# Kernel optimization log

Hardware: AMD Instinct MI355X
Metric: run time of the kernel (lower is better)

The kernel has to match this reference:

```python
import jax, jax.numpy as jnp
import numpy as np

DIM = 512
NUM_HEADS = 8
HEAD_DIM = DIM // NUM_HEADS
GAMMA = 1.0


def setup_inputs() -> dict:
    key = jax.random.key(0)
    ks = jax.random.split(key, 10)
    B, S = 2, 2048
    x_real = jax.random.normal(ks[0], (B, S, DIM), dtype=jnp.float32)
    x_imag = jax.random.normal(ks[1], (B, S, DIM), dtype=jnp.float32)
    def xavier(k, fan_in, fan_out):
        lim = float(np.sqrt(6.0 / (fan_in + fan_out)))
        return jax.random.uniform(k, (fan_in, fan_out), jnp.float32, -lim, lim)
    # torch Linear(in,out): weight [out,in]; we store transposed [in,out]
    Wq = xavier(ks[2], 2 * DIM, DIM); bq = jnp.zeros((DIM,), jnp.float32)
    Wk = xavier(ks[3], 2 * DIM, DIM); bk = jnp.zeros((DIM,), jnp.float32)
    Wv = xavier(ks[4], 2 * DIM, DIM); bv = jnp.zeros((DIM,), jnp.float32)
    Wo = xavier(ks[5], DIM, 2 * DIM); bo = jnp.zeros((2 * DIM,), jnp.float32)
    return {"x_real": x_real, "x_imag": x_imag, "Wq": Wq, "bq": bq,
            "Wk": Wk, "bk": bk, "Wv": Wv, "bv": bv, "Wo": Wo, "bo": bo}


def reference(x_real, x_imag, Wq, bq, Wk, bk, Wv, bv, Wo, bo):
    B, S, _ = x_real.shape
    real_embed = jnp.concatenate([x_real, x_imag], axis=-1)  # [B,S,2*dim]
    def proj(W, b):
        y = real_embed @ W + b                               # [B,S,dim]
        return y.reshape(B, S, NUM_HEADS, HEAD_DIM).transpose(0, 2, 1, 3)  # [B,H,S,d]
    Q = proj(Wq, bq)
    K = proj(Wk, bk)
    V = proj(Wv, bv)
    # softmax over head_dim is broadcast-invariant, so the Bhattacharyya
    # coefficient sum_d sqrt(p_i[d]*q_j[d]) factorizes into a matmul.
    sp = jnp.sqrt(jax.nn.softmax(Q, axis=-1))  # [B,H,S,d]
    sq = jnp.sqrt(jax.nn.softmax(K, axis=-1))  # [B,H,S,d]
    bc = jnp.einsum('bhid,bhjd->bhij', sp, sq)  # Bhattacharyya coeff [B,H,S,S]
    bc = jnp.clip(bc, -1.0, 1.0)
    dist = jnp.arccos(bc)
    attn = jax.nn.softmax(-GAMMA * dist * dist, axis=-1)  # [B,H,S,S]
    attended = jnp.einsum('bhij,bhjd->bhid', attn, V)
    attended = attended.transpose(0, 2, 1, 3).reshape(B, S, DIM)
    out = attended @ Wo + bo  # [B,S,2*dim] = concat(real_out, imag_out)
    return out
```

## Files before the change

### kernel.cpp

```cpp
#include <hip/hip_runtime.h>
#include <math.h>


typedef __attribute__((ext_vector_type(8))) short short8;
typedef __attribute__((ext_vector_type(4))) short bf16x4;
typedef __attribute__((ext_vector_type(4))) float f32x4;
typedef __attribute__((ext_vector_type(2))) float f32x2;

#define MFMA(a, b, c) __builtin_amdgcn_mfma_f32_16x16x32_bf16((a), (b), (c), 0, 0, 0)

static __device__ __forceinline__ short f2bf(float f) {
    unsigned u = __float_as_uint(f);
    u += 0x7fffu + ((u >> 16) & 1u);
    return (short)(u >> 16);
}

static __device__ __forceinline__ void gld_lds16(const short* g, short* l) {
    __builtin_amdgcn_global_load_lds(
        (const __attribute__((address_space(1))) unsigned int*)g,
        (__attribute__((address_space(3))) unsigned int*)l, 16, 0, 0);
}

__global__ __launch_bounds__(256) void convert_x(
    const float* __restrict__ xr, const float* __restrict__ xi,
    short* __restrict__ xb)
{
    int idx = blockIdx.x * 256 + threadIdx.x;
    int e = idx << 2;
    int m = e >> 10, k = e & 1023;
    const float* src = (k < 512) ? xr : xi;
    float4 t = *(const float4*)(src + (size_t)m * 512 + (k & 511));
    unsigned lo = (unsigned short)f2bf(t.x) | ((unsigned)(unsigned short)f2bf(t.y) << 16);
    unsigned hi = (unsigned short)f2bf(t.z) | ((unsigned)(unsigned short)f2bf(t.w) << 16);
    uint2 o; o.x = lo; o.y = hi;
    *(uint2*)(xb + e) = o;
}

__global__ __launch_bounds__(256) void transpose_w(
    const float* __restrict__ Wq, const float* __restrict__ Wk,
    const float* __restrict__ Wv, const float* __restrict__ Wo,
    short* __restrict__ wqt, short* __restrict__ wkt,
    short* __restrict__ wvt, short* __restrict__ wot)
{
    __shared__ float t[32][33];
    const int z = blockIdx.z;
    const float* src = (z == 0) ? Wq : (z == 1) ? Wk : (z == 2) ? Wv : Wo;
    short* dst = (z == 0) ? wqt : (z == 1) ? wkt : (z == 2) ? wvt : wot;
    const int K = (z < 3) ? 1024 : 512;
    const int N = (z < 3) ? 512 : 1024;
    const int n0 = blockIdx.x << 5, k0 = blockIdx.y << 5;
    if (n0 >= N || k0 >= K) return;
    const int tx = threadIdx.x & 31, ty = threadIdx.x >> 5;
    #pragma unroll
    for (int i = 0; i < 4; ++i)
        t[ty + 8 * i][tx] = src[(size_t)(k0 + ty + 8 * i) * N + n0 + tx];
    __syncthreads();
    #pragma unroll
    for (int i = 0; i < 4; ++i)
        dst[(size_t)(n0 + ty + 8 * i) * K + k0 + tx] = f2bf(t[tx][ty + 8 * i]);
}

__global__ __launch_bounds__(128, 4) void qkv_mfma(
    const short* __restrict__ xb, const short* __restrict__ wcat,
    const float* __restrict__ bq, const float* __restrict__ bk,
    const float* __restrict__ bv,
    short* __restrict__ sp, short* __restrict__ sq, short* __restrict__ vt)
{
    __shared__ short As[2][128 * 32];
    __shared__ short Bs[2][64 * 32];
    const int jb = blockIdx.x;
    const int m0 = blockIdx.y << 7;
    const int tid = threadIdx.x;
    const int w = tid >> 6, lane = tid & 63;
    const int l = lane & 15, quad = lane >> 4;

    const int srow = lane >> 2;
    const int sseg = (lane & 3) << 3;
    const short* gA = xb   + (size_t)(m0        + (w << 6) + srow) * 1024 + sseg;
    const short* gB = wcat + (size_t)((jb << 6) + (w << 5) + srow) * 1024 + sseg;

    #pragma unroll
    for (int t = 0; t < 4; ++t)
        gld_lds16(gA + t * 16 * 1024, &As[0][((w << 2) + t) << 9]);
    #pragma unroll
    for (int t = 0; t < 2; ++t)
        gld_lds16(gB + t * 16 * 1024, &Bs[0][((w << 1) + t) << 9]);
    __syncthreads();

    const f32x4 z4 = {0.f, 0.f, 0.f, 0.f};
    f32x4 acc[4][4];
    #pragma unroll
    for (int i = 0; i < 4; ++i)
        #pragma unroll
        for (int j = 0; j < 4; ++j) acc[i][j] = z4;

    for (int kt = 0; kt < 32; ++kt) {
        const int cb = kt & 1, nb = cb ^ 1;
        if (kt < 31) {
            const int k0 = (kt + 1) << 5;
            #pragma unroll
            for (int t = 0; t < 4; ++t)
                gld_lds16(gA + k0 + t * 16 * 1024, &As[nb][((w << 2) + t) << 9]);
            #pragma unroll
            for (int t = 0; t < 2; ++t)
                gld_lds16(gB + k0 + t * 16 * 1024, &Bs[nb][((w << 1) + t) << 9]);
        }
        const short* Al = &As[cb][(w << 6) << 5];
        const short* Bl = &Bs[cb][0];
        short8 af[4], bfr[4];
        #pragma unroll
        for (int i = 0; i < 4; ++i)
            af[i] = *(const short8*)(Al + (((i << 4) + l) << 5) + (quad << 3));
        #pragma unroll
        for (int j = 0; j < 4; ++j)
            bfr[j] = *(const short8*)(Bl + (((j << 4) + l) << 5) + (quad << 3));
        #pragma unroll
        for (int i = 0; i < 4; ++i)
            #pragma unroll
            for (int j = 0; j < 4; ++j)
                acc[i][j] = MFMA(af[i], bfr[j], acc[i][j]);
        __syncthreads();
    }

    const int op = jb >> 3;
    const int h  = jb & 7;

    if (op < 2) {
        short* dst = (op == 0) ? sp : sq;
        const float* bias = (op == 0) ? bq : bk;
        float bcol[4];
        #pragma unroll
        for (int nt = 0; nt < 4; ++nt) bcol[nt] = bias[(h << 6) + (nt << 4) + l];
        #pragma unroll
        for (int i = 0; i < 4; ++i) {
            #pragma unroll
            for (int reg = 0; reg < 4; ++reg) {
                const int r = m0 + (w << 6) + (i << 4) + (quad << 2) + reg;
                const int b = r >> 11, s = r & 2047;
                float v[4];
                #pragma unroll
                for (int nt = 0; nt < 4; ++nt) v[nt] = acc[i][nt][reg] + bcol[nt];
                float mx = fmaxf(fmaxf(v[0], v[1]), fmaxf(v[2], v[3]));
                #pragma unroll
                for (int msk = 1; msk < 16; msk <<= 1) mx = fmaxf(mx, __shfl_xor(mx, msk));
                float e[4], ssum = 0.f;
                #pragma unroll
                for (int nt = 0; nt < 4; ++nt) { e[nt] = __expf(v[nt] - mx); ssum += e[nt]; }
                #pragma unroll
                for (int msk = 1; msk < 16; msk <<= 1) ssum += __shfl_xor(ssum, msk);
                float inv = 1.0f / ssum;
                short* o = dst + ((size_t)((b << 3) + h) * 2048 + s) * 64 + l;
                #pragma unroll
                for (int nt = 0; nt < 4; ++nt)
                    o[nt << 4] = f2bf(sqrtf(e[nt] * inv));
            }
        }
    } else {
        float bcol[4];
        #pragma unroll
        for (int nt = 0; nt < 4; ++nt) bcol[nt] = bv[(h << 6) + (nt << 4) + l];
        #pragma unroll
        for (int i = 0; i < 4; ++i) {
            const int sb = m0 + (w << 6) + (i << 4) + (quad << 2);
            const int b = sb >> 11, s = sb & 2047;
            #pragma unroll
            for (int nt = 0; nt < 4; ++nt) {
                const int d = (nt << 4) + l;
                bf16x4 pk;
                #pragma unroll
                for (int reg = 0; reg < 4; ++reg)
                    pk[reg] = f2bf(acc[i][nt][reg] + bcol[nt]);
                *(bf16x4*)(vt + ((size_t)((b << 3) + h) * 64 + d) * 2048 + s) = pk;
            }
        }
    }
}

__global__ __launch_bounds__(256, 4) void attn_mfma(
    const short* __restrict__ sp, const short* __restrict__ sq,
    const short* __restrict__ vt, short* __restrict__ attB)
{
    __shared__ __align__(16) short sqT[2][64 * 64];
    __shared__ __align__(16) short vtT[2][64 * 64];
    __shared__ __align__(16) short Pb[4][16 * 64];
    __shared__ float denB[4][16];
    const int bh = blockIdx.y;
    const int m0 = blockIdx.x << 6;
    const int tid = threadIdx.x;
    const int w = tid >> 6, lane = tid & 63;
    const int l = lane & 15, quad = lane >> 4;
    const int l7 = l & 7;

    const short* spB = sp + (size_t)bh * 2048 * 64;
    const short* sqB = sq + (size_t)bh * 2048 * 64;
    const short* vtB = vt + (size_t)bh * 64 * 2048;

    const short* apr = spB + (size_t)(m0 + w * 16 + l) * 64 + quad * 8;
    short8 aq0 = *(const short8*)(apr);
    short8 aq1 = *(const short8*)(apr + 32);
    short8 nq0 = aq0 ^ (short)0x8000;
    short8 nq1 = aq1 ^ (short)0x8000;

    const int srow = tid >> 2;
    const int scol = (tid & 3) * 16;
    const short* sqG = sqB + (size_t)srow * 64 + scol;
    const short* vtG = vtB + (size_t)srow * 2048 + scol;
    const int sl0 = (tid & 3) << 1;
    const int sw0 = srow * 64 + (((sl0    ) ^ (srow & 7)) << 3);
    const int sw1 = srow * 64 + (((sl0 | 1) ^ (srow & 7)) << 3);

    const int sRd = (quad ^ l7) << 3;

    {
        short8 a0 = *(const short8*)(sqG);
        short8 a1 = *(const short8*)(sqG + 8);
        short8 b0 = *(const short8*)(vtG);
        short8 b1 = *(const short8*)(vtG + 8);
        *(short8*)(&sqT[0][sw0]) = a0;
        *(short8*)(&sqT[0][sw1]) = a1;
        *(short8*)(&vtT[0][sw0]) = b0;
        *(short8*)(&vtT[0][sw1]) = b1;
    }
    __syncthreads();

    const f32x4 z4 = {0.f, 0.f, 0.f, 0.f};
    const f32x4 ones4 = {1.f, 1.f, 1.f, 1.f};
    f32x4 acc[4] = {z4, z4, z4, z4};
    f32x2 den2 = {0.f, 0.f};
    short* Pw = &Pb[w][0];

    #pragma unroll 1
    for (int jt = 0; jt < 32; ++jt) {
        const int cb = jt & 1, nb = cb ^ 1;
        const int j0n = ((jt + 1) & 31) << 6;
        short8 na0 = *(const short8*)(sqG + (size_t)j0n * 64);
        short8 na1 = *(const short8*)(sqG + (size_t)j0n * 64 + 8);
        short8 nb0 = *(const short8*)(vtG + j0n);
        short8 nb1 = *(const short8*)(vtG + j0n + 8);

        const short* sqL = &sqT[cb][0];
        #pragma unroll
        for (int nt = 0; nt < 4; ++nt) {
            const short* ar = sqL + ((nt * 16 + l) << 6);
            short8 sa0 = *(const short8*)(ar + sRd);
            short8 sa1 = *(const short8*)(ar + (sRd ^ 32));
            f32x4 p = MFMA(sa0, nq0, ones4);
            p = MFMA(sa1, nq1, p);
            f32x2 u01 = {p[0], p[1]};
            f32x2 u23 = {p[2], p[3]};
            const f32x2 zz = {0.f, 0.f};
#if __has_builtin(__builtin_elementwise_max)
            u01 = __builtin_elementwise_max(u01, zz);
            u23 = __builtin_elementwise_max(u23, zz);
#else
            u01.x = fmaxf(u01.x, 0.f); u01.y = fmaxf(u01.y, 0.f);
            u23.x = fmaxf(u23.x, 0.f); u23.y = fmaxf(u23.y, 0.f);
#endif
            f32x2 t01 = {0.000922f, 0.000922f};
            f32x2 t23 = t01;
            t01 = t01 * u01 + 0.00152228f;  t23 = t23 * u23 + 0.00152228f;
            t01 = t01 * u01 + 0.00384801f;  t23 = t23 * u23 + 0.00384801f;
            t01 = t01 * u01 + 0.01015873f;  t23 = t23 * u23 + 0.01015873f;
            t01 = t01 * u01 + 0.02857143f;  t23 = t23 * u23 + 0.02857143f;
            t01 = t01 * u01 + 0.08888889f;  t23 = t23 * u23 + 0.08888889f;
            t01 = t01 * u01 + 0.33333333f;  t23 = t23 * u23 + 0.33333333f;
            t01 = t01 * u01 + 2.0f;         t23 = t23 * u23 + 2.0f;
            f32x2 w01 = u01 * t01;
            f32x2 w23 = u23 * t23;
            float e0 = __expf(-w01.x), e1 = __expf(-w01.y);
            float e2 = __expf(-w23.x), e3 = __expf(-w23.y);
            f32x2 es = {e0 + e2, e1 + e3};
            den2 += es;
            uint2 pk;
            pk.x = (__float_as_uint(e0) >> 16) | (__float_as_uint(e1) & 0xffff0000u);
            pk.y = (__float_as_uint(e2) >> 16) | (__float_as_uint(e3) & 0xffff0000u);
            *(uint2*)(&Pw[(l << 6) + ((((nt << 1) + (quad >> 1)) ^ l7) << 3)
                          + ((quad & 1) << 2)]) = pk;
        }

        const short* pr = Pw + (l << 6);
        short8 pa0 = *(const short8*)(pr + sRd);
        short8 pa1 = *(const short8*)(pr + (sRd ^ 32));
        const short* vL = &vtT[cb][0];
        #pragma unroll
        for (int t4 = 0; t4 < 4; ++t4) {
            const short* vr = vL + ((t4 * 16 + l) << 6);
            short8 vb0 = *(const short8*)(vr + sRd);
            short8 vb1 = *(const short8*)(vr + (sRd ^ 32));
            acc[t4] = MFMA(pa0, vb0, acc[t4]);
            acc[t4] = MFMA(pa1, vb1, acc[t4]);
        }

        *(short8*)(&sqT[nb][sw0]) = na0;
        *(short8*)(&sqT[nb][sw1]) = na1;
        *(short8*)(&vtT[nb][sw0]) = nb0;
        *(short8*)(&vtT[nb][sw1]) = nb1;
        __syncthreads();
    }

    float den = den2.x + den2.y;
    den += __shfl_xor(den, 16);
    den += __shfl_xor(den, 32);
    if (lane < 16) denB[w][l] = den;
    float invd[4];
    #pragma unroll
    for (int reg = 0; reg < 4; ++reg)
        invd[reg] = 1.0f / denB[w][quad * 4 + reg];

    const int b = bh >> 3, hh = bh & 7;
    #pragma unroll
    for (int t4 = 0; t4 < 4; ++t4)
        #pragma unroll
        for (int reg = 0; reg < 4; ++reg) {
            const int row = m0 + w * 16 + quad * 4 + reg;
            attB[((size_t)(b * 2048 + row)) * 512 + hh * 64 + t4 * 16 + l] =
                f2bf(acc[t4][reg] * invd[reg]);
        }
}

__global__ __launch_bounds__(256, 3) void out_mfma(
    const short* __restrict__ attB, const short* __restrict__ wot,
    const float* __restrict__ bo, float* __restrict__ out)
{
    __shared__ short As[2][128 * 32];
    __shared__ short Bs[2][64 * 32];
    const int nb0 = blockIdx.x << 6;
    const int m0 = blockIdx.y << 7;
    const int tid = threadIdx.x;
    const int w = tid >> 6, lane = tid & 63;
    const int l = lane & 15, quad = lane >> 4;

    const short* gA = attB + (size_t)(m0  + (w << 4) + (lane >> 2)) * 512 + ((lane & 3) << 3);
    const short* gB = wot  + (size_t)(nb0 + (w << 4) + (lane >> 2)) * 512 + ((lane & 3) << 3);

    gld_lds16(gA,            &As[0][w << 9]);
    gld_lds16(gA + 64 * 512, &As[0][(w + 4) << 9]);
    gld_lds16(gB,            &Bs[0][w << 9]);
    __syncthreads();

    const f32x4 z4 = {0.f, 0.f, 0.f, 0.f};
    f32x4 acc[4][2];
    #pragma unroll
    for (int i = 0; i < 4; ++i) { acc[i][0] = z4; acc[i][1] = z4; }

    const int rsel = (w >> 1) << 6;
    const int csel = (w & 1) << 5;

    for (int kt = 0; kt < 16; ++kt) {
        const int cb = kt & 1, nbuf = cb ^ 1;
        if (kt < 15) {
            const int k0 = (kt + 1) << 5;
            gld_lds16(gA + k0,            &As[nbuf][w << 9]);
            gld_lds16(gA + k0 + 64 * 512, &As[nbuf][(w + 4) << 9]);
            gld_lds16(gB + k0,            &Bs[nbuf][w << 9]);
        }
        const short* Al = &As[cb][rsel << 5];
        const short* Bl = &Bs[cb][csel << 5];
        short8 af[4], bfr[2];
        #pragma unroll
        for (int i = 0; i < 4; ++i)
            af[i] = *(const short8*)(Al + (((i << 4) + l) << 5) + (quad << 3));
        #pragma unroll
        for (int j = 0; j < 2; ++j)
            bfr[j] = *(const short8*)(Bl + (((j << 4) + l) << 5) + (quad << 3));
        #pragma unroll
        for (int i = 0; i < 4; ++i) {
            acc[i][0] = MFMA(af[i], bfr[0], acc[i][0]);
            acc[i][1] = MFMA(af[i], bfr[1], acc[i][1]);
        }
        __syncthreads();
    }

    const int n0 = nb0 + csel;
    float bcol[2];
    bcol[0] = bo[n0 + l];
    bcol[1] = bo[n0 + 16 + l];
    #pragma unroll
    for (int i = 0; i < 4; ++i)
        #pragma unroll
        for (int reg = 0; reg < 4; ++reg) {
            const int m = m0 + rsel + (i << 4) + (quad << 2) + reg;
            float* o = out + (size_t)m * 1024 + n0 + l;
            o[0]  = acc[i][0][reg] + bcol[0];
            o[16] = acc[i][1][reg] + bcol[1];
        }
}

extern "C" void kernel_launch(void* const* d_in, const int* in_sizes, int n_in,
                              void* d_out, int out_size, void* d_ws, size_t ws_size,
                              hipStream_t stream) {
    const float* xr = (const float*)d_in[0];
    const float* xi = (const float*)d_in[1];
    const float* Wq = (const float*)d_in[2];
    const float* bq = (const float*)d_in[3];
    const float* Wk = (const float*)d_in[4];
    const float* bk = (const float*)d_in[5];
    const float* Wv = (const float*)d_in[6];
    const float* bv = (const float*)d_in[7];
    const float* Wo = (const float*)d_in[8];
    const float* bo = (const float*)d_in[9];
    float* out = (float*)d_out;

    short* base = (short*)d_ws;
    short* xb   = base;
    short* wqt  = xb  + 4194304;
    short* wkt  = wqt + 524288;
    short* wvt  = wkt + 524288;
    short* wot  = wvt + 524288;
    short* spW  = wot + 524288;
    short* sqW  = spW + 2097152;
    short* vtW  = sqW + 2097152;
    short* attB = vtW + 2097152;

    hipLaunchKernelGGL(convert_x, dim3(4096), dim3(256), 0, stream, xr, xi, xb);
    hipLaunchKernelGGL(transpose_w, dim3(32, 32, 4), dim3(256), 0, stream,
                       Wq, Wk, Wv, Wo, wqt, wkt, wvt, wot);
    hipLaunchKernelGGL(qkv_mfma, dim3(24, 32), dim3(128), 0, stream,
                       xb, wqt, bq, bk, bv, spW, sqW, vtW);
    hipLaunchKernelGGL(attn_mfma, dim3(32, 16), dim3(256), 0, stream,
                       spW, sqW, vtW, attB);
    hipLaunchKernelGGL(out_mfma, dim3(16, 32), dim3(256), 0, stream,
                       attB, wot, bo, out);
}
```

Baseline: 185.7 us.

## Triple-buffer LDS staging in QKV and output GEMMs with partial vmcnt waits

Both projection GEMMs move from double to triple-buffered global-to-LDS loads. Each iteration issues loads two k-tiles ahead and waits only for the older batch (vmcnt) before a raw barrier, instead of a full __syncthreads drain. The goal is to hide global load latency behind MFMA work. It raises LDS use per block, which may reduce occupancy. It also issues wasted wrap-around loads in the last two iterations and relies on hand-counted vmcnt values being correct.

New measurement: 185.5 us. No clear change (-0.1%).

```diff
diff --git a/kernel.cpp b/kernel.cpp
--- a/kernel.cpp
+++ b/kernel.cpp
@@ -66,8 +66,8 @@
     const float* __restrict__ bv,
     short* __restrict__ sp, short* __restrict__ sq, short* __restrict__ vt)
 {
-    __shared__ short As[2][128 * 32];
-    __shared__ short Bs[2][64 * 32];
+    __shared__ short As[3][128 * 32];
+    __shared__ short Bs[3][64 * 32];
     const int jb = blockIdx.x;
     const int m0 = blockIdx.y << 7;
     const int tid = threadIdx.x;
@@ -79,13 +79,20 @@
     const short* gA = xb   + (size_t)(m0        + (w << 6) + srow) * 1024 + sseg;
     const short* gB = wcat + (size_t)((jb << 6) + (w << 5) + srow) * 1024 + sseg;
 
-    #pragma unroll
-    for (int t = 0; t < 4; ++t)
-        gld_lds16(gA + t * 16 * 1024, &As[0][((w << 2) + t) << 9]);
-    #pragma unroll
-    for (int t = 0; t < 2; ++t)
-        gld_lds16(gB + t * 16 * 1024, &Bs[0][((w << 1) + t) << 9]);
-    __syncthreads();
+    auto STAGE = [&](int bb, int kk) {
+        const int k0 = kk << 5;
+        #pragma unroll
+        for (int t = 0; t < 4; ++t)
+            gld_lds16(gA + k0 + t * 16 * 1024, &As[bb][((w << 2) + t) << 9]);
+        #pragma unroll
+        for (int t = 0; t < 2; ++t)
+            gld_lds16(gB + k0 + t * 16 * 1024, &Bs[bb][((w << 1) + t) << 9]);
+    };
+
+    STAGE(0, 0);
+    STAGE(1, 1);
+    asm volatile("s_waitcnt vmcnt(6)" ::: "memory");
+    __builtin_amdgcn_s_barrier();
 
     const f32x4 z4 = {0.f, 0.f, 0.f, 0.f};
     f32x4 acc[4][4];
@@ -94,17 +101,10 @@
         #pragma unroll
         for (int j = 0; j < 4; ++j) acc[i][j] = z4;
 
+    int cb = 0, sb = 2;
+    #pragma unroll 1
     for (int kt = 0; kt < 32; ++kt) {
-        const int cb = kt & 1, nb = cb ^ 1;
-        if (kt < 31) {
-            const int k0 = (kt + 1) << 5;
-            #pragma unroll
-            for (int t = 0; t < 4; ++t)
-                gld_lds16(gA + k0 + t * 16 * 1024, &As[nb][((w << 2) + t) << 9]);
-            #pragma unroll
-            for (int t = 0; t < 2; ++t)
-                gld_lds16(gB + k0 + t * 16 * 1024, &Bs[nb][((w << 1) + t) << 9]);
-        }
+        STAGE(sb, (kt + 2) & 31);
         const short* Al = &As[cb][(w << 6) << 5];
         const short* Bl = &Bs[cb][0];
         short8 af[4], bfr[4];
@@ -119,8 +119,12 @@
             #pragma unroll
             for (int j = 0; j < 4; ++j)
                 acc[i][j] = MFMA(af[i], bfr[j], acc[i][j]);
-        __syncthreads();
+        asm volatile("s_waitcnt vmcnt(6)" ::: "memory");
+        __builtin_amdgcn_s_barrier();
+        cb = (cb == 2) ? 0 : cb + 1;
+        sb = (sb == 2) ? 0 : sb + 1;
     }
+    asm volatile("s_waitcnt vmcnt(0)" ::: "memory");
 
     const int op = jb >> 3;
     const int h  = jb & 7;
@@ -161,8 +165,8 @@
         for (int nt = 0; nt < 4; ++nt) bcol[nt] = bv[(h << 6) + (nt << 4) + l];
         #pragma unroll
         for (int i = 0; i < 4; ++i) {
-            const int sb = m0 + (w << 6) + (i << 4) + (quad << 2);
-            const int b = sb >> 11, s = sb & 2047;
+            const int sb2 = m0 + (w << 6) + (i << 4) + (quad << 2);
+            const int b = sb2 >> 11, s = sb2 & 2047;
             #pragma unroll
             for (int nt = 0; nt < 4; ++nt) {
                 const int d = (nt << 4) + l;
@@ -322,8 +326,8 @@
     const short* __restrict__ attB, const short* __restrict__ wot,
     const float* __restrict__ bo, float* __restrict__ out)
 {
-    __shared__ short As[2][128 * 32];
-    __shared__ short Bs[2][64 * 32];
+    __shared__ short As[3][128 * 32];
+    __shared__ short Bs[3][64 * 32];
     const int nb0 = blockIdx.x << 6;
     const int m0 = blockIdx.y << 7;
     const int tid = threadIdx.x;
@@ -333,10 +337,17 @@
     const short* gA = attB + (size_t)(m0  + (w << 4) + (lane >> 2)) * 512 + ((lane & 3) << 3);
     const short* gB = wot  + (size_t)(nb0 + (w << 4) + (lane >> 2)) * 512 + ((lane & 3) << 3);
 
-    gld_lds16(gA,            &As[0][w << 9]);
-    gld_lds16(gA + 64 * 512, &As[0][(w + 4) << 9]);
-    gld_lds16(gB,            &Bs[0][w << 9]);
-    __syncthreads();
+    auto STAGE = [&](int bb, int kk) {
+        const int k0 = kk << 5;
+        gld_lds16(gA + k0,            &As[bb][w << 9]);
+        gld_lds16(gA + k0 + 64 * 512, &As[bb][(w + 4) << 9]);
+        gld_lds16(gB + k0,            &Bs[bb][w << 9]);
+    };
+
+    STAGE(0, 0);
+    STAGE(1, 1);
+    asm volatile("s_waitcnt vmcnt(3)" ::: "memory");
+    __builtin_amdgcn_s_barrier();
 
     const f32x4 z4 = {0.f, 0.f, 0.f, 0.f};
     f32x4 acc[4][2];
@@ -346,14 +357,10 @@
     const int rsel = (w >> 1) << 6;
     const int csel = (w & 1) << 5;
 
+    int cb = 0, sb = 2;
+    #pragma unroll 1
     for (int kt = 0; kt < 16; ++kt) {
-        const int cb = kt & 1, nbuf = cb ^ 1;
-        if (kt < 15) {
-            const int k0 = (kt + 1) << 5;
-            gld_lds16(gA + k0,            &As[nbuf][w << 9]);
-            gld_lds16(gA + k0 + 64 * 512, &As[nbuf][(w + 4) << 9]);
-            gld_lds16(gB + k0,            &Bs[nbuf][w << 9]);
-        }
+        STAGE(sb, (kt + 2) & 15);
         const short* Al = &As[cb][rsel << 5];
         const short* Bl = &Bs[cb][csel << 5];
         short8 af[4], bfr[2];
@@ -368,8 +375,12 @@
             acc[i][0] = MFMA(af[i], bfr[0], acc[i][0]);
             acc[i][1] = MFMA(af[i], bfr[1], acc[i][1]);
         }
-        __syncthreads();
+        asm volatile("s_waitcnt vmcnt(3)" ::: "memory");
+        __builtin_amdgcn_s_barrier();
+        cb = (cb == 2) ? 0 : cb + 1;
+        sb = (sb == 2) ? 0 : sb + 1;
     }
+    asm volatile("s_waitcnt vmcnt(0)" ::: "memory");
 
     const int n0 = nb0 + csel;
     float bcol[2];
```
